# Kernel tuning notes

Hardware: AMD Instinct MI355X
Metric: run time of the kernel (lower is better)

## Reference

```python
import jax, jax.numpy as jnp
import numpy as np

ALPHA = 0.5      # sklearn Lasso(alpha=0.5)
N_ITERS = 50     # fixed FISTA iterations
N_POWER = 10     # power iterations for Lipschitz estimate


def _soft(x, thr):
    return jnp.sign(x) * jnp.maximum(jnp.abs(x) - thr, 0.0)


def setup_inputs() -> dict:
    key = jax.random.key(0)
    k1, k2 = jax.random.split(key)
    B, n_rx, n_tx, n_carrier = 8, 4, 32, 256
    M = 256
    D = n_rx * n_tx * n_carrier * 2  # 65536
    x = jax.random.normal(k1, (B, n_rx, n_tx, n_carrier, 2), jnp.float32)
    coding_mat = jax.random.normal(k2, (B, M, D), jnp.float32)
    return {"x": x, "coding_mat": coding_mat}


def _lasso_fista(x, coding_mat):
    B = x.shape[0]
    M = coding_mat.shape[1]
    D = coding_mat.shape[2]
    shape = x.shape
    w_true = x.reshape(B, D)                       # (nrx ntx channel complex) flatten
    y = jnp.einsum('bmd,bd->bm', coding_mat, w_true)  # compressed measurements

    # Lipschitz constant of grad of (1/(2M))||y - Aw||^2 via power iteration on A^T A / M
    def power_step(_, v):
        Av = jnp.einsum('bmd,bd->bm', coding_mat, v)
        v = jnp.einsum('bmd,bm->bd', coding_mat, Av)
        return v / (jnp.linalg.norm(v, axis=-1, keepdims=True) + 1e-12)

    v = jnp.full((B, D), 1.0 / np.sqrt(D), dtype=x.dtype)
    v = jax.lax.fori_loop(0, N_POWER, power_step, v)
    Av = jnp.einsum('bmd,bd->bm', coding_mat, v)
    L = jnp.einsum('bm,bm->b', Av, Av) / M        # rayleigh quotient, v unit norm
    L = jax.lax.stop_gradient(L)[:, None]          # [B,1] step-size constant

    w0 = jnp.zeros((B, D), x.dtype)

    def fista_step(carry, _):
        w, z, t = carry
        r = jnp.einsum('bmd,bd->bm', coding_mat, z) - y
        grad = jnp.einsum('bmd,bm->bd', coding_mat, r) / M
        w_new = _soft(z - grad / L, ALPHA / L)
        t_new = 0.5 * (1.0 + jnp.sqrt(1.0 + 4.0 * t * t))
        z_new = w_new + ((t - 1.0) / t_new) * (w_new - w)
        return (w_new, z_new, t_new), None

    (w, _, _), _ = jax.lax.scan(fista_step, (w0, w0, jnp.float32(1.0)), None, length=N_ITERS)
    return w.reshape(shape)


def reference(x, coding_mat):
    return _lasso_fista(x, coding_mat)
```

## Files before the change

### kernel.cpp

```cpp
#include <hip/hip_runtime.h>
#include <hip/hip_fp16.h>
#include <math.h>

#define B 8
#define M 256
#define D 65536
#define NCH 512

static constexpr float ALPHA = 0.5f;
static constexpr int N_ITERS = 50;
static constexpr int N_POWER = 10;

typedef _Float16 f16x8 __attribute__((ext_vector_type(8)));
typedef float f32x4 __attribute__((ext_vector_type(4)));


__global__ __launch_bounds__(256) void k_conv_y(const float* __restrict__ A,
                                                const float* __restrict__ x,
                                                __half* __restrict__ Aht,
                                                float* __restrict__ ypart,
                                                float* __restrict__ upart) {
    const size_t n8 = (size_t)B * M * D / 8;
    size_t stride = (size_t)gridDim.x * 256;
    for (size_t i = (size_t)blockIdx.x * 256 + threadIdx.x; i < n8; i += stride) {
        size_t dlo8 = i & 15;
        size_t m  = (i >> 4) & (M - 1);
        size_t ch = (i >> 12) & (NCH - 1);
        size_t b  = i >> 21;
        size_t in8 = (b << 21) | (m << 13) | (ch << 4) | dlo8;
        float4 f0 = ((const float4*)A)[2 * in8];
        float4 f1 = ((const float4*)A)[2 * in8 + 1];
        union { uint4 u; __half2 h[4]; } o;
        o.h[0] = __floats2half2_rn(f0.x, f0.y);
        o.h[1] = __floats2half2_rn(f0.z, f0.w);
        o.h[2] = __floats2half2_rn(f1.x, f1.y);
        o.h[3] = __floats2half2_rn(f1.z, f1.w);
        ((uint4*)Aht)[i] = o.u;

        const float4* xp =
            (const float4*)(x + ((b << 16) | (ch << 7) | (dlo8 << 3)));
        float4 x0 = xp[0], x1 = xp[1];
        float2 g0 = __half22float2(o.h[0]);
        float2 g1 = __half22float2(o.h[1]);
        float2 g2 = __half22float2(o.h[2]);
        float2 g3 = __half22float2(o.h[3]);
        float p = g0.x * x0.x + g0.y * x0.y + g1.x * x0.z + g1.y * x0.w +
                  g2.x * x1.x + g2.y * x1.y + g3.x * x1.z + g3.y * x1.w;
        float q = g0.x + g0.y + g1.x + g1.y + g2.x + g2.y + g3.x + g3.y;
        p += __shfl_xor(p, 1, 64); q += __shfl_xor(q, 1, 64);
        p += __shfl_xor(p, 2, 64); q += __shfl_xor(q, 2, 64);
        p += __shfl_xor(p, 4, 64); q += __shfl_xor(q, 4, 64);
        p += __shfl_xor(p, 8, 64); q += __shfl_xor(q, 8, 64);
        if (dlo8 == 0) {
            ypart[i >> 4] = p;
            upart[i >> 4] = q;
        }
    }
}

__global__ __launch_bounds__(256) void k_yred(const float* __restrict__ ypart,
                                              const float* __restrict__ upart,
                                              float* __restrict__ y,
                                              float* __restrict__ u) {
    int blk = blockIdx.x;
    int b = blk >> 3;
    int mg = blk & 7;
    int t = threadIdx.x;
    int tm = t & 31;
    int cg = t >> 5;
    int m = mg * 32 + tm;
    const float* yp = ypart + (size_t)b * NCH * M + m;
    const float* up = upart + (size_t)b * NCH * M + m;
    float sy = 0.f, su = 0.f;
#pragma unroll 8
    for (int ch = cg; ch < NCH; ch += 8) {
        sy += yp[(size_t)ch * M];
        su += up[(size_t)ch * M];
    }
    __shared__ float redY[8][32], redU[8][32];
    redY[cg][tm] = sy; redU[cg][tm] = su;
    __syncthreads();
    if (t < 32) {
        float vy = 0.f, vu = 0.f;
#pragma unroll
        for (int g = 0; g < 8; ++g) { vy += redY[g][t]; vu += redU[g][t]; }
        int bm = b * M + mg * 32 + t;
        y[bm] = vy;
        u[bm] = vu * 0.00390625f;
    }
}

__global__ __launch_bounds__(256) void k_gram_mfma(const __half* __restrict__ Aht,
                                                   float* __restrict__ G) {
    int bx = blockIdx.x;
    int ch2 = bx & 31;
    int p  = (bx >> 5) % 3;
    int b  = bx / 96;
    const int PI[3] = {0, 0, 128};
    const int PJ[3] = {0, 128, 128};
    int ti = PI[p], tj = PJ[p];
    int k0 = ch2 * 2048;

    __shared__ __half As[128 * 32];
    __shared__ __half Bs[128 * 32];

    int t = threadIdx.x;
    int w = t >> 6, lane = t & 63;
    int wr = w >> 1, wc = w & 1;

    int srow = w * 32 + (lane >> 2);
    int scol = (lane & 3) * 8;

    f32x4 acc[4][4];
#pragma unroll
    for (int i = 0; i < 4; ++i)
#pragma unroll
        for (int j = 0; j < 4; ++j)
            acc[i][j] = (f32x4){0.f, 0.f, 0.f, 0.f};

    int frow = lane & 15;
    int koff = (lane >> 4) * 8;

    const size_t bbase = (size_t)b * NCH;
    for (int ks = 0; ks < 2048; ks += 32) {
        int d = k0 + ks;
        size_t chb = bbase + (d >> 7);
        int dlo = d & 127;
        __syncthreads();
        {
            const __half* ga0 = Aht + (chb * M + (ti + srow)) * 128 + dlo + scol;
            const __half* ga1 = ga0 + 16 * 128;
            const __half* gb0 = Aht + (chb * M + (tj + srow)) * 128 + dlo + scol;
            const __half* gb1 = gb0 + 16 * 128;
            __builtin_amdgcn_global_load_lds(
                (const __attribute__((address_space(1))) void*)ga0,
                (__attribute__((address_space(3))) void*)&As[(w * 32) * 32], 16, 0, 0);
            __builtin_amdgcn_global_load_lds(
                (const __attribute__((address_space(1))) void*)ga1,
                (__attribute__((address_space(3))) void*)&As[(w * 32 + 16) * 32], 16, 0, 0);
            __builtin_amdgcn_global_load_lds(
                (const __attribute__((address_space(1))) void*)gb0,
                (__attribute__((address_space(3))) void*)&Bs[(w * 32) * 32], 16, 0, 0);
            __builtin_amdgcn_global_load_lds(
                (const __attribute__((address_space(1))) void*)gb1,
                (__attribute__((address_space(3))) void*)&Bs[(w * 32 + 16) * 32], 16, 0, 0);
        }
        __syncthreads();

        f16x8 aF[4], bF[4];
#pragma unroll
        for (int i = 0; i < 4; ++i)
            aF[i] = *(const f16x8*)&As[(wr * 64 + i * 16 + frow) * 32 + koff];
#pragma unroll
        for (int j = 0; j < 4; ++j)
            bF[j] = *(const f16x8*)&Bs[(wc * 64 + j * 16 + frow) * 32 + koff];
#pragma unroll
        for (int i = 0; i < 4; ++i)
#pragma unroll
            for (int j = 0; j < 4; ++j)
                acc[i][j] = __builtin_amdgcn_mfma_f32_16x16x32_f16(
                    aF[i], bF[j], acc[i][j], 0, 0, 0);
    }

    float* Gb = G + (size_t)b * M * M;
    bool offd = (ti != tj);
    int r0 = (lane >> 4) * 4;
    int c0 = lane & 15;
#pragma unroll
    for (int i = 0; i < 4; ++i)
#pragma unroll
        for (int j = 0; j < 4; ++j)
#pragma unroll
            for (int r = 0; r < 4; ++r) {
                int gi = ti + wr * 64 + i * 16 + r0 + r;
                int gj = tj + wc * 64 + j * 16 + c0;
                float v = acc[i][j][r];
                atomicAdd(&Gb[(size_t)gi * M + gj], v);
                if (offd) atomicAdd(&Gb[(size_t)gj * M + gi], v);
            }
}

__global__ __launch_bounds__(256) void k_power(const float* __restrict__ G,
                                               const float* __restrict__ u0,
                                               float* __restrict__ Lp) {
    int b = blockIdx.x;
    int m = threadIdx.x;
    __shared__ float su[M];
    __shared__ float red[4];
    su[m] = u0[b * M + m];
    __syncthreads();
    const float* Gb = G + (size_t)b * M * M;
    for (int it = 0; it < N_POWER; ++it) {
        float gm = 0.f;
        const float4* grow = (const float4*)(Gb + (size_t)m * M);
#pragma unroll 8
        for (int k = 0; k < M / 4; ++k) {
            float4 g = grow[k];
            gm += g.x * su[4 * k] + g.y * su[4 * k + 1] + g.z * su[4 * k + 2] +
                  g.w * su[4 * k + 3];
        }
        float part = su[m] * gm;
        for (int off = 32; off > 0; off >>= 1) part += __shfl_down(part, off, 64);
        if ((m & 63) == 0) red[m >> 6] = part;
        __syncthreads();
        float n = sqrtf(red[0] + red[1] + red[2] + red[3]);
        float inv = 1.f / (n + 1e-12f);
        su[m] = gm * inv;
        __syncthreads();
    }
    float part = su[m] * su[m];
    for (int off = 32; off > 0; off >>= 1) part += __shfl_down(part, off, 64);
    if ((m & 63) == 0) red[m >> 6] = part;
    __syncthreads();
    if (m == 0) {
        float L = (red[0] + red[1] + red[2] + red[3]) * (1.0f / 256.0f);
        Lp[b * 4 + 0] = L;
        Lp[b * 4 + 1] = 1.0f / (256.0f * L);
        Lp[b * 4 + 2] = ALPHA / L;
    }
}

__global__ __launch_bounds__(256) void k_cstep(const float* __restrict__ spart,
                                               const float* __restrict__ y,
                                               const float* __restrict__ Lp,
                                               float* __restrict__ c) {
    int blk = blockIdx.x;
    int b = blk >> 3;
    int mg = blk & 7;
    int t = threadIdx.x;
    int tm = t & 31;
    int cg = t >> 5;
    int m = mg * 32 + tm;
    const float* sp = spart + (size_t)b * NCH * M + m;
    float s = 0.f;
#pragma unroll 8
    for (int ch = cg; ch < NCH; ch += 8)
        s += sp[(size_t)ch * M];
    __shared__ float red[8][32];
    red[cg][tm] = s;
    __syncthreads();
    if (t < 32) {
        float sv = red[0][t] + red[1][t] + red[2][t] + red[3][t] +
                   red[4][t] + red[5][t] + red[6][t] + red[7][t];
        int bm = b * M + mg * 32 + t;
        c[bm] = (sv - y[bm]) * Lp[b * 4 + 1];
    }
}

__global__ __launch_bounds__(256) void k_fista(const __half* __restrict__ Aht,
                                               const float* __restrict__ cc,
                                               const float* __restrict__ Lp,
                                               float* __restrict__ z,
                                               float* __restrict__ w,
                                               float* __restrict__ spart,
                                               float beta) {
    int cid = blockIdx.x;
    int b = cid >> 8;
    int pair = cid & 255;
    int t = threadIdx.x;
    int dj = t & 15;
    int mi = t >> 4;

    __shared__ float sc[M];
    __shared__ float gws[4][16][8];
    __shared__ float znS[128];
    __shared__ float sred[M];

    sc[t] = cc[b * M + t];
    __syncthreads();
    float thr = Lp[b * 4 + 2];

    for (int half = 0; half < 2; ++half) {
        int chunk = pair * 2 + half;
        int d0 = chunk << 7;

        const __half* Ap =
            Aht + (((size_t)b * NCH + chunk) * M + mi) * 128 + dj * 8;
        uint4 areg[16];
        float g[8] = {};
#pragma unroll
        for (int s = 0; s < 16; ++s) {
            areg[s] = *(const uint4*)(Ap + (size_t)(s * 16) * 128);
            float cm = sc[s * 16 + mi];
            const __half2* hp = (const __half2*)&areg[s];
            float2 f0 = __half22float2(hp[0]);
            float2 f1 = __half22float2(hp[1]);
            float2 f2 = __half22float2(hp[2]);
            float2 f3 = __half22float2(hp[3]);
            g[0] = fmaf(f0.x, cm, g[0]); g[1] = fmaf(f0.y, cm, g[1]);
            g[2] = fmaf(f1.x, cm, g[2]); g[3] = fmaf(f1.y, cm, g[3]);
            g[4] = fmaf(f2.x, cm, g[4]); g[5] = fmaf(f2.y, cm, g[5]);
            g[6] = fmaf(f3.x, cm, g[6]); g[7] = fmaf(f3.y, cm, g[7]);
        }
#pragma unroll
        for (int j = 0; j < 8; ++j) {
            g[j] += __shfl_xor(g[j], 16, 64);
            g[j] += __shfl_xor(g[j], 32, 64);
        }
        int wv = t >> 6;
        if ((t & 63) < 16) {
#pragma unroll
            for (int j = 0; j < 8; ++j) gws[wv][dj][j] = g[j];
        }
        __syncthreads();

        if (t < 128) {
            int ldj = t >> 3, lj = t & 7;
            float gs = gws[0][ldj][lj] + gws[1][ldj][lj] +
                       gws[2][ldj][lj] + gws[3][ldj][lj];
            size_t zi = (size_t)b * D + d0 + t;
            float zv = z[zi], wold = w[zi];
            float cand = zv - gs;
            float a1 = fabsf(cand) - thr;
            float wn = a1 > 0.f ? copysignf(a1, cand) : 0.f;
            float znv = wn + beta * (wn - wold);
            w[zi] = wn;
            z[zi] = znv;
            znS[t] = znv;
        }
        __syncthreads();

        float zr[8];
        {
            float4 z0 = *(const float4*)&znS[dj * 8];
            float4 z1 = *(const float4*)&znS[dj * 8 + 4];
            zr[0] = z0.x; zr[1] = z0.y; zr[2] = z0.z; zr[3] = z0.w;
            zr[4] = z1.x; zr[5] = z1.y; zr[6] = z1.z; zr[7] = z1.w;
        }
#pragma unroll
        for (int s = 0; s < 16; ++s) {
            const __half2* hp = (const __half2*)&areg[s];
            float2 f0 = __half22float2(hp[0]);
            float2 f1 = __half22float2(hp[1]);
            float2 f2 = __half22float2(hp[2]);
            float2 f3 = __half22float2(hp[3]);
            float p = f0.x * zr[0] + f0.y * zr[1] + f1.x * zr[2] +
                      f1.y * zr[3] + f2.x * zr[4] + f2.y * zr[5] +
                      f3.x * zr[6] + f3.y * zr[7];
            p += __shfl_xor(p, 1, 64);
            p += __shfl_xor(p, 2, 64);
            p += __shfl_xor(p, 4, 64);
            p += __shfl_xor(p, 8, 64);
            if (dj == 0) sred[s * 16 + mi] = p;
        }
        __syncthreads();
        spart[((size_t)b * NCH + chunk) * M + t] = sred[t];
    }
}

extern "C" void kernel_launch(void* const* d_in, const int* in_sizes, int n_in,
                              void* d_out, int out_size, void* d_ws, size_t ws_size,
                              hipStream_t stream) {
    (void)in_sizes; (void)n_in; (void)out_size; (void)ws_size;
    const float* x = (const float*)d_in[0];
    const float* A = (const float*)d_in[1];
    float* w = (float*)d_out;

    __half* Aht = (__half*)d_ws;
    float* ws = (float*)((char*)d_ws + (size_t)B * M * D * sizeof(__half));
    float* y  = ws;
    float* u  = ws + 2048;
    float* Lp = ws + 4096;
    float* c  = ws + 4128;
    float* z  = ws + 8192;
    float* G  = ws + 8192 + 524288;
    float* spart = G;
    float* ypart = spart + (size_t)B * NCH * M;
    float* upart = ypart + (size_t)B * NCH * M;

    hipMemsetAsync(G, 0, (size_t)B * M * M * sizeof(float), stream);
    hipMemsetAsync(z, 0, (size_t)B * D * sizeof(float), stream);
    hipMemsetAsync(w, 0, (size_t)B * D * sizeof(float), stream);

    k_conv_y<<<16384, 256, 0, stream>>>(A, x, Aht, ypart, upart);
    k_yred<<<64, 256, 0, stream>>>(ypart, upart, y, u);
    k_gram_mfma<<<8 * 3 * 32, 256, 0, stream>>>(Aht, G);
    k_power<<<B, 256, 0, stream>>>(G, u, Lp);

    hipMemsetAsync(spart, 0, (size_t)B * NCH * M * sizeof(float), stream);

    double t = 1.0;
    for (int k = 0; k < N_ITERS; ++k) {
        double tn = 0.5 * (1.0 + sqrt(1.0 + 4.0 * t * t));
        float beta = (float)((t - 1.0) / tn);
        k_cstep<<<64, 256, 0, stream>>>(spart, y, Lp, c);
        k_fista<<<2048, 256, 0, stream>>>(Aht, c, Lp, z, w, spart, beta);
        t = tn;
    }
}
```

Before: 3.965 ms.

## Fuse residual reduction into FISTA kernel via atomics and triple-buffered accumulators

Removes the separate k_cstep reduction kernel per iteration. Each FISTA block now atomically adds its partial A·z into a global accumulator, and the next iteration reads that accumulator directly to form the residual. Three rotating buffers (read, zero, write) avoid a memset between iterations. The grid also changes from 2048 blocks of two chunks each to 4096 blocks of one chunk. The cost is 256 atomics per block plus a redundant residual computation in every block, in exchange for 50 fewer launches and no spart round-trip.

```diff
diff --git a/kernel.cpp b/kernel.cpp
--- a/kernel.cpp
+++ b/kernel.cpp
@@ -220,43 +220,17 @@
     }
 }
 
-__global__ __launch_bounds__(256) void k_cstep(const float* __restrict__ spart,
+__global__ __launch_bounds__(256) void k_fista(const __half* __restrict__ Aht,
                                                const float* __restrict__ y,
-                                               const float* __restrict__ Lp,
-                                               float* __restrict__ c) {
-    int blk = blockIdx.x;
-    int b = blk >> 3;
-    int mg = blk & 7;
-    int t = threadIdx.x;
-    int tm = t & 31;
-    int cg = t >> 5;
-    int m = mg * 32 + tm;
-    const float* sp = spart + (size_t)b * NCH * M + m;
-    float s = 0.f;
-#pragma unroll 8
-    for (int ch = cg; ch < NCH; ch += 8)
-        s += sp[(size_t)ch * M];
-    __shared__ float red[8][32];
-    red[cg][tm] = s;
-    __syncthreads();
-    if (t < 32) {
-        float sv = red[0][t] + red[1][t] + red[2][t] + red[3][t] +
-                   red[4][t] + red[5][t] + red[6][t] + red[7][t];
-        int bm = b * M + mg * 32 + t;
-        c[bm] = (sv - y[bm]) * Lp[b * 4 + 1];
-    }
-}
-
-__global__ __launch_bounds__(256) void k_fista(const __half* __restrict__ Aht,
-                                               const float* __restrict__ cc,
                                                const float* __restrict__ Lp,
                                                float* __restrict__ z,
                                                float* __restrict__ w,
-                                               float* __restrict__ spart,
-                                               float beta) {
+                                               float* __restrict__ sacc,
+                                               int it, float beta) {
     int cid = blockIdx.x;
-    int b = cid >> 8;
-    int pair = cid & 255;
+    int b = cid >> 9;
+    int chunk = cid & (NCH - 1);
+    int d0 = chunk << 7;
     int t = threadIdx.x;
     int dj = t & 15;
     int mi = t >> 4;
@@ -266,86 +240,85 @@
     __shared__ float znS[128];
     __shared__ float sred[M];
 
-    sc[t] = cc[b * M + t];
-    __syncthreads();
-    float thr = Lp[b * 4 + 2];
-
-    for (int half = 0; half < 2; ++half) {
-        int chunk = pair * 2 + half;
-        int d0 = chunk << 7;
-
-        const __half* Ap =
-            Aht + (((size_t)b * NCH + chunk) * M + mi) * 128 + dj * 8;
-        uint4 areg[16];
-        float g[8] = {};
-#pragma unroll
-        for (int s = 0; s < 16; ++s) {
-            areg[s] = *(const uint4*)(Ap + (size_t)(s * 16) * 128);
-            float cm = sc[s * 16 + mi];
-            const __half2* hp = (const __half2*)&areg[s];
-            float2 f0 = __half22float2(hp[0]);
-            float2 f1 = __half22float2(hp[1]);
-            float2 f2 = __half22float2(hp[2]);
-            float2 f3 = __half22float2(hp[3]);
-            g[0] = fmaf(f0.x, cm, g[0]); g[1] = fmaf(f0.y, cm, g[1]);
-            g[2] = fmaf(f1.x, cm, g[2]); g[3] = fmaf(f1.y, cm, g[3]);
-            g[4] = fmaf(f2.x, cm, g[4]); g[5] = fmaf(f2.y, cm, g[5]);
-            g[6] = fmaf(f3.x, cm, g[6]); g[7] = fmaf(f3.y, cm, g[7]);
-        }
-#pragma unroll
-        for (int j = 0; j < 8; ++j) {
-            g[j] += __shfl_xor(g[j], 16, 64);
-            g[j] += __shfl_xor(g[j], 32, 64);
-        }
-        int wv = t >> 6;
-        if ((t & 63) < 16) {
-#pragma unroll
-            for (int j = 0; j < 8; ++j) gws[wv][dj][j] = g[j];
-        }
-        __syncthreads();
-
-        if (t < 128) {
-            int ldj = t >> 3, lj = t & 7;
-            float gs = gws[0][ldj][lj] + gws[1][ldj][lj] +
-                       gws[2][ldj][lj] + gws[3][ldj][lj];
-            size_t zi = (size_t)b * D + d0 + t;
-            float zv = z[zi], wold = w[zi];
-            float cand = zv - gs;
-            float a1 = fabsf(cand) - thr;
-            float wn = a1 > 0.f ? copysignf(a1, cand) : 0.f;
-            float znv = wn + beta * (wn - wold);
-            w[zi] = wn;
-            z[zi] = znv;
-            znS[t] = znv;
-        }
-        __syncthreads();
-
-        float zr[8];
-        {
-            float4 z0 = *(const float4*)&znS[dj * 8];
-            float4 z1 = *(const float4*)&znS[dj * 8 + 4];
-            zr[0] = z0.x; zr[1] = z0.y; zr[2] = z0.z; zr[3] = z0.w;
-            zr[4] = z1.x; zr[5] = z1.y; zr[6] = z1.z; zr[7] = z1.w;
-        }
-#pragma unroll
-        for (int s = 0; s < 16; ++s) {
-            const __half2* hp = (const __half2*)&areg[s];
-            float2 f0 = __half22float2(hp[0]);
-            float2 f1 = __half22float2(hp[1]);
-            float2 f2 = __half22float2(hp[2]);
-            float2 f3 = __half22float2(hp[3]);
-            float p = f0.x * zr[0] + f0.y * zr[1] + f1.x * zr[2] +
-                      f1.y * zr[3] + f2.x * zr[4] + f2.y * zr[5] +
-                      f3.x * zr[6] + f3.y * zr[7];
-            p += __shfl_xor(p, 1, 64);
-            p += __shfl_xor(p, 2, 64);
-            p += __shfl_xor(p, 4, 64);
-            p += __shfl_xor(p, 8, 64);
-            if (dj == 0) sred[s * 16 + mi] = p;
-        }
-        __syncthreads();
-        spart[((size_t)b * NCH + chunk) * M + t] = sred[t];
-    }
+    const float* sread = sacc + (size_t)((it + 2) % 3) * B * M;
+    float* szero = sacc + (size_t)((it + 1) % 3) * B * M;
+    float* swrt  = sacc + (size_t)(it % 3) * B * M;
+
+    int bm = b * M + t;
+    sc[t] = (sread[bm] - y[bm]) * Lp[b * 4 + 1];
+    if (chunk == 0) szero[bm] = 0.f;
+    __syncthreads();
+
+    const __half* Ap = Aht + (((size_t)b * NCH + chunk) * M + mi) * 128 + dj * 8;
+    uint4 areg[16];
+    float g[8] = {};
+#pragma unroll
+    for (int s = 0; s < 16; ++s) {
+        areg[s] = *(const uint4*)(Ap + (size_t)(s * 16) * 128);
+        float cm = sc[s * 16 + mi];
+        const __half2* hp = (const __half2*)&areg[s];
+        float2 f0 = __half22float2(hp[0]);
+        float2 f1 = __half22float2(hp[1]);
+        float2 f2 = __half22float2(hp[2]);
+        float2 f3 = __half22float2(hp[3]);
+        g[0] = fmaf(f0.x, cm, g[0]); g[1] = fmaf(f0.y, cm, g[1]);
+        g[2] = fmaf(f1.x, cm, g[2]); g[3] = fmaf(f1.y, cm, g[3]);
+        g[4] = fmaf(f2.x, cm, g[4]); g[5] = fmaf(f2.y, cm, g[5]);
+        g[6] = fmaf(f3.x, cm, g[6]); g[7] = fmaf(f3.y, cm, g[7]);
+    }
+#pragma unroll
+    for (int j = 0; j < 8; ++j) {
+        g[j] += __shfl_xor(g[j], 16, 64);
+        g[j] += __shfl_xor(g[j], 32, 64);
+    }
+    int wv = t >> 6;
+    if ((t & 63) < 16) {
+#pragma unroll
+        for (int j = 0; j < 8; ++j) gws[wv][dj][j] = g[j];
+    }
+    __syncthreads();
+
+    if (t < 128) {
+        int ldj = t >> 3, lj = t & 7;
+        float gs = gws[0][ldj][lj] + gws[1][ldj][lj] +
+                   gws[2][ldj][lj] + gws[3][ldj][lj];
+        size_t zi = (size_t)b * D + d0 + t;
+        float thr = Lp[b * 4 + 2];
+        float zv = z[zi], wold = w[zi];
+        float cand = zv - gs;
+        float a1 = fabsf(cand) - thr;
+        float wn = a1 > 0.f ? copysignf(a1, cand) : 0.f;
+        float znv = wn + beta * (wn - wold);
+        w[zi] = wn;
+        z[zi] = znv;
+        znS[t] = znv;
+    }
+    __syncthreads();
+
+    float zr[8];
+    {
+        float4 z0 = *(const float4*)&znS[dj * 8];
+        float4 z1 = *(const float4*)&znS[dj * 8 + 4];
+        zr[0] = z0.x; zr[1] = z0.y; zr[2] = z0.z; zr[3] = z0.w;
+        zr[4] = z1.x; zr[5] = z1.y; zr[6] = z1.z; zr[7] = z1.w;
+    }
+#pragma unroll
+    for (int s = 0; s < 16; ++s) {
+        const __half2* hp = (const __half2*)&areg[s];
+        float2 f0 = __half22float2(hp[0]);
+        float2 f1 = __half22float2(hp[1]);
+        float2 f2 = __half22float2(hp[2]);
+        float2 f3 = __half22float2(hp[3]);
+        float p = f0.x * zr[0] + f0.y * zr[1] + f1.x * zr[2] + f1.y * zr[3] +
+                  f2.x * zr[4] + f2.y * zr[5] + f3.x * zr[6] + f3.y * zr[7];
+        p += __shfl_xor(p, 1, 64);
+        p += __shfl_xor(p, 2, 64);
+        p += __shfl_xor(p, 4, 64);
+        p += __shfl_xor(p, 8, 64);
+        if (dj == 0) sred[s * 16 + mi] = p;
+    }
+    __syncthreads();
+    atomicAdd(&swrt[bm], sred[t]);
 }
 
 extern "C" void kernel_launch(void* const* d_in, const int* in_sizes, int n_in,
@@ -361,30 +334,27 @@
     float* y  = ws;
     float* u  = ws + 2048;
     float* Lp = ws + 4096;
-    float* c  = ws + 4128;
     float* z  = ws + 8192;
     float* G  = ws + 8192 + 524288;
-    float* spart = G;
-    float* ypart = spart + (size_t)B * NCH * M;
+    float* ypart = G + 524288;
     float* upart = ypart + (size_t)B * NCH * M;
+    float* sacc  = upart + (size_t)B * NCH * M;
 
     hipMemsetAsync(G, 0, (size_t)B * M * M * sizeof(float), stream);
     hipMemsetAsync(z, 0, (size_t)B * D * sizeof(float), stream);
     hipMemsetAsync(w, 0, (size_t)B * D * sizeof(float), stream);
+    hipMemsetAsync(sacc, 0, 3 * B * M * sizeof(float), stream);
 
     k_conv_y<<<16384, 256, 0, stream>>>(A, x, Aht, ypart, upart);
     k_yred<<<64, 256, 0, stream>>>(ypart, upart, y, u);
     k_gram_mfma<<<8 * 3 * 32, 256, 0, stream>>>(Aht, G);
     k_power<<<B, 256, 0, stream>>>(G, u, Lp);
 
-    hipMemsetAsync(spart, 0, (size_t)B * NCH * M * sizeof(float), stream);
-
     double t = 1.0;
     for (int k = 0; k < N_ITERS; ++k) {
         double tn = 0.5 * (1.0 + sqrt(1.0 + 4.0 * t * t));
         float beta = (float)((t - 1.0) / tn);
-        k_cstep<<<64, 256, 0, stream>>>(spart, y, Lp, c);
-        k_fista<<<2048, 256, 0, stream>>>(Aht, c, Lp, z, w, spart, beta);
+        k_fista<<<B * NCH, 256, 0, stream>>>(Aht, y, Lp, z, w, sacc, k, beta);
         t = tn;
     }
 }
```

Measured after the change: 4.501 ms. 1.14x slower.
